# Performance work log

Measured on AMD Instinct MI355X. Metric: run time of the kernel, lower is better.

Reference implementation:

```python
import jax, jax.numpy as jnp
import numpy as np

D_MODEL = 1024
N_HEADS = 16
HEAD_DIM = D_MODEL // N_HEADS
D_FF = 4096
BATCH = 4
SEQ = 2048
LN_EPS = 1e-5


def layer_norm(x, g, b):
    mu = jnp.mean(x, axis=-1, keepdims=True)
    var = jnp.mean(jnp.square(x - mu), axis=-1, keepdims=True)
    return (x - mu) * jax.lax.rsqrt(var + LN_EPS) * g + b


def setup_inputs() -> dict:
    key = jax.random.key(0)
    ks = jax.random.split(key, 8)
    s = 0.02
    x = jax.random.normal(ks[0], (BATCH, SEQ, D_MODEL), jnp.float32)
    mask = jnp.triu(jnp.ones((SEQ, SEQ), dtype=bool), k=1)  # True = masked
    return {
        "x": x,
        "ln1_g": jnp.ones((D_MODEL,), jnp.float32),
        "ln1_b": jnp.zeros((D_MODEL,), jnp.float32),
        "qkv_w": jax.random.normal(ks[1], (3 * D_MODEL, D_MODEL), jnp.float32) * s,
        "qkv_b": jnp.zeros((3 * D_MODEL,), jnp.float32),
        "out_w": jax.random.normal(ks[2], (D_MODEL, D_MODEL), jnp.float32) * s,
        "out_b": jnp.zeros((D_MODEL,), jnp.float32),
        "ln2_g": jnp.ones((D_MODEL,), jnp.float32),
        "ln2_b": jnp.zeros((D_MODEL,), jnp.float32),
        "fc1_w": jax.random.normal(ks[3], (D_FF, D_MODEL), jnp.float32) * s,
        "fc1_b": jnp.zeros((D_FF,), jnp.float32),
        "fc2_w": jax.random.normal(ks[4], (D_MODEL, D_FF), jnp.float32) * s,
        "fc2_b": jnp.zeros((D_MODEL,), jnp.float32),
        "mask": mask,
    }


def reference(x, ln1_g, ln1_b, qkv_w, qkv_b, out_w, out_b,
              ln2_g, ln2_b, fc1_w, fc1_b, fc2_w, fc2_b, mask):
    b, s, _ = x.shape
    # --- pre-norm attention ---
    h = layer_norm(x, ln1_g, ln1_b)
    qkv = h @ qkv_w.T + qkv_b                       # [b, s, 3*D]
    qkv = qkv.reshape(b, s, 3, N_HEADS, HEAD_DIM)
    q, k, v = (jnp.moveaxis(qkv[:, :, i], 2, 1) for i in range(3))  # [b, H, s, hd]
    scale = HEAD_DIM ** -0.5
    attn = jnp.einsum('bhqd,bhkd->bhqk', q, k) * scale
    attn = jnp.where(mask, -jnp.inf, attn)
    attn = jax.nn.softmax(attn, axis=-1)
    o = jnp.einsum('bhqk,bhkd->bhqd', attn, v)      # [b, H, s, hd]
    o = jnp.moveaxis(o, 1, 2).reshape(b, s, D_MODEL)
    x = x + (o @ out_w.T + out_b)
    # --- pre-norm FFN ---
    h = layer_norm(x, ln2_g, ln2_b)
    h = jax.nn.gelu(h @ fc1_w.T + fc1_b, approximate=False)
    x = x + (h @ fc2_w.T + fc2_b)
    return x
```

## Files before the change

### kernel.cpp

```cpp
#include <hip/hip_runtime.h>
#include <math.h>

using u16 = unsigned short;
typedef __attribute__((ext_vector_type(8))) short short8;
typedef __attribute__((ext_vector_type(4))) float f32x4;
typedef __attribute__((ext_vector_type(16))) float f32x16;
typedef __attribute__((ext_vector_type(4))) u16 u16x4;

#define DEV __device__ __forceinline__

DEV u16 f2bf(float f) {
    unsigned u = __float_as_uint(f);
    u += 0x7fffu + ((u >> 16) & 1u);
    return (u16)(u >> 16);
}
DEV float bf2f(u16 h) { return __uint_as_float(((unsigned)h) << 16); }

DEV short8 ld16(const u16* p) { return *reinterpret_cast<const short8*>(p); }

DEV float gelu_f(float x) {
    const float u = x * (0.7978845608f + 0.0356774081f * x * x);
    const float e = __builtin_amdgcn_exp2f(u * 2.885390082f);
    const float t = 1.f - 2.f * __builtin_amdgcn_rcpf(e + 1.f);
    return 0.5f * x * (1.f + t);
}

DEV unsigned pk2(float a, float b) {
    unsigned r;
    asm("v_cvt_pk_bf16_f32 %0, %1, %2" : "=v"(r) : "v"(a), "v"(b));
    return r;
}

#define GLL16(gp, lp)                                                          \
    __builtin_amdgcn_global_load_lds(                                          \
        (const __attribute__((address_space(1))) void*)(gp),                   \
        (__attribute__((address_space(3))) void*)(lp), 16, 0, 0)

#define VMC(n) asm volatile("s_waitcnt vmcnt(" #n ")" ::: "memory")
#define LGKM0() asm volatile("s_waitcnt lgkmcnt(0)" ::: "memory")

__global__ void cvt_f32_bf16(const float* __restrict__ in, u16* __restrict__ out, int n4) {
    int i = blockIdx.x * 256 + threadIdx.x;
    if (i >= n4) return;
    float4 v = reinterpret_cast<const float4*>(in)[i];
    u16x4 o;
    o.x = f2bf(v.x); o.y = f2bf(v.y); o.z = f2bf(v.z); o.w = f2bf(v.w);
    reinterpret_cast<u16x4*>(out)[i] = o;
}

__global__ __launch_bounds__(256) void ln_bf16(const float* __restrict__ x,
                                               const float* __restrict__ gm,
                                               const float* __restrict__ bt,
                                               u16* __restrict__ out) {
    const int row = blockIdx.x, tid = threadIdx.x;
    const float4 v = reinterpret_cast<const float4*>(x + (long)row * 1024)[tid];
    float s  = v.x + v.y + v.z + v.w;
    float sq = v.x * v.x + v.y * v.y + v.z * v.z + v.w * v.w;
#pragma unroll
    for (int off = 1; off <= 32; off <<= 1) {
        s  += __shfl_xor(s, off);
        sq += __shfl_xor(sq, off);
    }
    __shared__ float ss[4], ssq[4];
    const int wave = tid >> 6, lane = tid & 63;
    if (lane == 0) { ss[wave] = s; ssq[wave] = sq; }
    __syncthreads();
    s  = ss[0] + ss[1] + ss[2] + ss[3];
    sq = ssq[0] + ssq[1] + ssq[2] + ssq[3];
    const float mu   = s * (1.f / 1024.f);
    const float var  = sq * (1.f / 1024.f) - mu * mu;
    const float rstd = rsqrtf(var + 1e-5f);
    const float4 g4 = reinterpret_cast<const float4*>(gm)[tid];
    const float4 b4 = reinterpret_cast<const float4*>(bt)[tid];
    u16x4 o;
    o.x = f2bf((v.x - mu) * rstd * g4.x + b4.x);
    o.y = f2bf((v.y - mu) * rstd * g4.y + b4.y);
    o.z = f2bf((v.z - mu) * rstd * g4.z + b4.z);
    o.w = f2bf((v.w - mu) * rstd * g4.w + b4.w);
    reinterpret_cast<u16x4*>(out + (long)row * 1024)[tid] = o;
}

#define TS(c, r) ((c) * 128 + (((((r) >> 3) ^ ((c) & 15))) << 3) + ((r) & 7))
#define CS(r, ck) ((r) * 128 + ((((ck) ^ ((r) & 15))) << 3))

template <int EPI, int BK>
__global__ __launch_bounds__(256, (BK == 32) ? 4 : 2) void gemm_bt(
    const u16* __restrict__ A, const u16* __restrict__ B,
    const float* __restrict__ bias, const float* res, float* outf,
    u16* __restrict__ outb, u16* __restrict__ Qb, u16* __restrict__ Kb,
    u16* __restrict__ Vtb, int M, int N, int K, int ldk) {
    constexpr int BUFU = (BK == 32) ? 8192 : 16384;
    __shared__ u16 shpool[2 * BUFU];

    const int tid = threadIdx.x;
    const int wave = tid >> 6, lane = tid & 63;
    const int lo = lane & 15, g = lane >> 4;
    const int wr = wave >> 1, wc = wave & 1;

    const int nwg = gridDim.x, chunk = nwg >> 3;
    const int wgid = (blockIdx.x & 7) * chunk + (blockIdx.x >> 3);
    const int nSmCol = N >> 10;
    const int s = wgid >> 6, w6 = wgid & 63;
    const int bm = (s / nSmCol) * 8 + (w6 >> 3);
    const int bn = (s % nSmCol) * 8 + (w6 & 7);
    const int row0 = bm * 128, col0 = bn * 128;

    const u16 *Ag, *Bg;
    if constexpr (BK == 32) {
        const int lrow = lane >> 2;
        const int lg   = (lane & 3) ^ ((lane >> 3) & 3);
        Ag = A + (long)(row0 + wave * 16 + lrow) * ldk + lg * 8;
        Bg = B + (long)(col0 + wave * 16 + lrow) * ldk + lg * 8;
    } else {
        const int lg = (lane & 7) ^ ((lane >> 3) & 7);
        Ag = A + (long)(row0 + wave * 32 + (lane >> 3)) * ldk + lg * 8;
        Bg = B + (long)(col0 + wave * 32 + (lane >> 3)) * ldk + lg * 8;
    }

    auto STAGE = [&](int tb, int kt) {
        if constexpr (BK == 32) {
            u16* Al = shpool + tb * 8192 + wave * 512;
            u16* Bl = Al + 4096;
            GLL16(Ag + (long)kt * 32, Al);
            GLL16(Ag + 64 * (long)ldk + (long)kt * 32, Al + 2048);
            GLL16(Bg + (long)kt * 32, Bl);
            GLL16(Bg + 64 * (long)ldk + (long)kt * 32, Bl + 2048);
        } else {
            u16* Al = shpool + tb * 16384 + wave * 2048;
            u16* Bl = Al + 8192;
            GLL16(Ag + (long)kt * 64,                  Al);
            GLL16(Ag + (long)kt * 64 +  8 * (long)ldk, Al + 512);
            GLL16(Ag + (long)kt * 64 + 16 * (long)ldk, Al + 1024);
            GLL16(Ag + (long)kt * 64 + 24 * (long)ldk, Al + 1536);
            GLL16(Bg + (long)kt * 64,                  Bl);
            GLL16(Bg + (long)kt * 64 +  8 * (long)ldk, Bl + 512);
            GLL16(Bg + (long)kt * 64 + 16 * (long)ldk, Bl + 1024);
            GLL16(Bg + (long)kt * 64 + 24 * (long)ldk, Bl + 1536);
        }
    };

    f32x4 acc[4][4] = {};

    STAGE(0, 0);
    STAGE(1, 1);

    const int T = K / BK;
    for (int t = 0; t < T; ++t) {
        const int cur = t & 1;
        if (t + 1 < T) {
            if constexpr (BK == 32) { VMC(4); } else { VMC(8); }
        } else { VMC(0); }
        __builtin_amdgcn_s_barrier();
        const u16* As = shpool + cur * BUFU;
        const u16* Bs = As + BUFU / 2;
        if constexpr (BK == 32) {
            short8 af[4], bfr[4];
            const int agp = g ^ ((lo >> 1) & 3);
#pragma unroll
            for (int m = 0; m < 4; ++m)
                af[m] = ld16(&As[(wr * 64 + m * 16 + lo) * 32 + agp * 8]);
#pragma unroll
            for (int n = 0; n < 4; ++n)
                bfr[n] = ld16(&Bs[(wc * 64 + n * 16 + lo) * 32 + agp * 8]);
            LGKM0();
            __builtin_amdgcn_s_barrier();
            if (t + 2 < T) STAGE(cur, t + 2);
#pragma unroll
            for (int m = 0; m < 4; ++m)
#pragma unroll
                for (int n = 0; n < 4; ++n)
                    acc[m][n] = __builtin_amdgcn_mfma_f32_16x16x32_bf16(
                        bfr[n], af[m], acc[m][n], 0, 0, 0);
        } else {
            short8 af[2][4], bfr[2][4];
#pragma unroll
            for (int ks = 0; ks < 2; ++ks) {
                const int ch = ((ks * 4 + g) ^ (lo & 7)) * 8;
#pragma unroll
                for (int m = 0; m < 4; ++m)
                    af[ks][m] = ld16(&As[(wr * 64 + m * 16 + lo) * 64 + ch]);
#pragma unroll
                for (int n = 0; n < 4; ++n)
                    bfr[ks][n] = ld16(&Bs[(wc * 64 + n * 16 + lo) * 64 + ch]);
            }
            LGKM0();
            __builtin_amdgcn_s_barrier();
            if (t + 2 < T) STAGE(cur, t + 2);
#pragma unroll
            for (int ks = 0; ks < 2; ++ks)
#pragma unroll
                for (int m = 0; m < 4; ++m)
#pragma unroll
                    for (int n = 0; n < 4; ++n)
                        acc[m][n] = __builtin_amdgcn_mfma_f32_16x16x32_bf16(
                            bfr[ks][n], af[ks][m], acc[m][n], 0, 0, 0);
        }
    }

    if constexpr (EPI == 1) {
#pragma unroll
        for (int n = 0; n < 4; ++n) {
            const int cb = col0 + wc * 64 + n * 16 + g * 4;
            const float4 b4 = *reinterpret_cast<const float4*>(&bias[cb]);
            const int ch = wc * 8 + n * 2 + (g >> 1);
#pragma unroll
            for (int m = 0; m < 4; ++m) {
                const int r = wr * 64 + m * 16 + lo;
                u16x4 o = {f2bf(gelu_f(acc[m][n][0] + b4.x)),
                           f2bf(gelu_f(acc[m][n][1] + b4.y)),
                           f2bf(gelu_f(acc[m][n][2] + b4.z)),
                           f2bf(gelu_f(acc[m][n][3] + b4.w))};
                *reinterpret_cast<u16x4*>(&shpool[CS(r, ch) + (g & 1) * 4]) = o;
            }
        }
        __syncthreads();
        const int row = tid >> 1, hl = tid & 1;
        u16* drow = outb + (long)(row0 + row) * N + col0 + hl * 64;
        const int rk = row & 15;
#pragma unroll
        for (int i = 0; i < 8; ++i) {
            const int ck = hl * 8 + i;
            *reinterpret_cast<short8*>(drow + i * 8) =
                *reinterpret_cast<const short8*>(&shpool[row * 128 + ((ck ^ rk) << 3)]);
        }
        return;
    }

    if constexpr (EPI == 3) {
        const int part = col0 >> 10;
        if (part == 2) {
            __syncthreads();
#pragma unroll
            for (int n = 0; n < 4; ++n) {
                const int cb = wc * 64 + n * 16 + g * 4;
                const float4 b4 = *reinterpret_cast<const float4*>(&bias[col0 + cb]);
#pragma unroll
                for (int m = 0; m < 4; ++m) {
                    const int rl = wr * 64 + m * 16 + lo;
                    shpool[TS(cb + 0, rl)] = f2bf(acc[m][n][0] + b4.x);
                    shpool[TS(cb + 1, rl)] = f2bf(acc[m][n][1] + b4.y);
                    shpool[TS(cb + 2, rl)] = f2bf(acc[m][n][2] + b4.z);
                    shpool[TS(cb + 3, rl)] = f2bf(acc[m][n][3] + b4.w);
                }
            }
            __syncthreads();
            const int c = tid >> 1, hlf = tid & 1;
            const int dcol = (col0 - 2048) + c;
            const int head = dcol >> 6, d = dcol & 63;
            const int bb = row0 >> 11;
            u16* dst = Vtb + ((long)(bb * 16 + head) * 64 + d) * 2048 +
                       (row0 & 2047) + hlf * 64;
            const u16* srcb = shpool + c * 128;
#pragma unroll
            for (int i = 0; i < 8; ++i) {
                const int pc = (hlf * 8 + i) ^ (c & 15);
                *reinterpret_cast<short8*>(dst + i * 8) =
                    *reinterpret_cast<const short8*>(srcb + pc * 8);
            }
            return;
        }
        const float qs = (part == 0) ? 0.18033688f : 1.0f;
#pragma unroll
        for (int n = 0; n < 4; ++n) {
            const int cb = col0 + wc * 64 + n * 16 + g * 4;
            const float4 b4 = *reinterpret_cast<const float4*>(&bias[cb]);
            const int ch = wc * 8 + n * 2 + (g >> 1);
#pragma unroll
            for (int m = 0; m < 4; ++m) {
                const int r = wr * 64 + m * 16 + lo;
                u16x4 o = {f2bf((acc[m][n][0] + b4.x) * qs),
                           f2bf((acc[m][n][1] + b4.y) * qs),
                           f2bf((acc[m][n][2] + b4.z) * qs),
                           f2bf((acc[m][n][3] + b4.w) * qs)};
                *reinterpret_cast<u16x4*>(&shpool[CS(r, ch) + (g & 1) * 4]) = o;
            }
        }
        __syncthreads();
        const int row = tid >> 1, hl = tid & 1;
        const int headbase = (col0 & 1023) >> 6;
        const int head = headbase + hl;
        const int bb = row0 >> 11;
        const int srow = (row0 & 2047) + row;
        u16* drow = (part == 0 ? Qb : Kb) +
                    ((long)(bb * 16 + head) * 2048 + srow) * 64;
        const int rk = row & 15;
#pragma unroll
        for (int i = 0; i < 8; ++i) {
            const int ck = hl * 8 + i;
            *reinterpret_cast<short8*>(drow + i * 8) =
                *reinterpret_cast<const short8*>(&shpool[row * 128 + ((ck ^ rk) << 3)]);
        }
        return;
    }

#pragma unroll
    for (int n = 0; n < 4; ++n) {
        const int cb = col0 + wc * 64 + n * 16 + g * 4;
        const float4 b4 = *reinterpret_cast<const float4*>(&bias[cb]);
#pragma unroll
        for (int m = 0; m < 4; ++m) {
            const int r = row0 + wr * 64 + m * 16 + lo;
            const float4 rr = *reinterpret_cast<const float4*>(&res[(long)r * N + cb]);
            float4 o = {rr.x + acc[m][n][0] + b4.x, rr.y + acc[m][n][1] + b4.y,
                        rr.z + acc[m][n][2] + b4.z, rr.w + acc[m][n][3] + b4.w};
            *reinterpret_cast<float4*>(&outf[(long)r * N + cb]) = o;
        }
    }
}

__global__ __launch_bounds__(256) void attn_fwd32(
    const u16* __restrict__ Q, const u16* __restrict__ K,
    const u16* __restrict__ Vt, u16* __restrict__ O) {
    __shared__ u16 kvl[2][8192];
    const int bh = blockIdx.x;
    const int strip = 15 - blockIdx.y;
    const int wave = threadIdx.x >> 6, lane = threadIdx.x & 63;
    const int lq = lane & 31, hi = lane >> 5;
    const int qw = strip * 128 + wave * 32;

    const u16* Kg = K + (long)bh * 2048 * 64;
    const u16* Vg = Vt + (long)bh * 64 * 2048;
    const int bb = bh >> 4, h = bh & 15;
    const u16* Qp = Q + ((long)bh * 2048 + qw) * 64;

    const int srow = wave * 8 + (lane >> 3);
    const int sc   = (lane & 7) ^ (srow & 7);

#define ASTAGE(b, kt) do {                                                     \
        const long kvb = (long)(kt) * 64;                                      \
        GLL16(Kg + (kvb + srow) * 64 + sc * 8,        &kvl[b][wave * 512]);    \
        GLL16(Kg + (kvb + 32 + srow) * 64 + sc * 8,   &kvl[b][2048 + wave * 512]); \
        GLL16(Vg + (long)srow * 2048 + kvb + sc * 8,  &kvl[b][4096 + wave * 512]); \
        GLL16(Vg + (long)(32 + srow) * 2048 + kvb + sc * 8,                    \
              &kvl[b][6144 + wave * 512]);                                     \
    } while (0)

    short8 qf[4];
#pragma unroll
    for (int ks = 0; ks < 4; ++ks)
        qf[ks] = ld16(Qp + lq * 64 + ks * 16 + hi * 8);

    f32x16 o0 = {}, o1 = {};
    float m = -1e30f, l = 0.f;
    const int q_abs = qw + lq;
    const int my_end = qw + 32;
    const int T = 2 * (strip + 1);
    const int swp = lq & 7;

    ASTAGE(0, 0);
    ASTAGE(1, 1);

    for (int t = 0; t < T; ++t) {
        const int cur = t & 1;
        const int kv0 = t * 64;
        if (t + 1 < T) { VMC(4); } else { VMC(0); }
        __builtin_amdgcn_s_barrier();
        const bool active = (kv0 < my_end);
        f32x16 s0 = {}, s1 = {};
        short8 vf0[4], vf1[4];
        if (active) {
            const u16* Kb = &kvl[cur][0];
            __builtin_amdgcn_s_setprio(1);
#pragma unroll
            for (int ks = 0; ks < 4; ++ks)
                s0 = __builtin_amdgcn_mfma_f32_32x32x16_bf16(
                    ld16(Kb + lq * 64 + ((ks * 2 + hi) ^ swp) * 8), qf[ks], s0, 0, 0, 0);
#pragma unroll
            for (int ks = 0; ks < 4; ++ks)
                s1 = __builtin_amdgcn_mfma_f32_32x32x16_bf16(
                    ld16(Kb + 2048 + lq * 64 + ((ks * 2 + hi) ^ swp) * 8), qf[ks], s1, 0, 0, 0);
            __builtin_amdgcn_s_setprio(0);
            const u16* Vb = &kvl[cur][4096];
#pragma unroll
            for (int c = 0; c < 4; ++c) {
                vf0[c] = ld16(Vb + lq * 64 + ((c * 2 + hi) ^ swp) * 8);
                vf1[c] = ld16(Vb + 2048 + lq * 64 + ((c * 2 + hi) ^ swp) * 8);
            }
        }
        LGKM0();
        __builtin_amdgcn_s_barrier();
        if (t + 2 < T) ASTAGE(cur, t + 2);
        if (active) {
            float mt = -1e30f;
            if (kv0 + 64 >= my_end) {
#pragma unroll
                for (int r = 0; r < 16; ++r) {
                    const int kv = kv0 + (r & 3) + 8 * (r >> 2) + 4 * hi;
                    if (kv > q_abs) s0[r] = -1e30f;
                    mt = fmaxf(mt, s0[r]);
                    if (kv + 32 > q_abs) s1[r] = -1e30f;
                    mt = fmaxf(mt, s1[r]);
                }
            } else {
#pragma unroll
                for (int r = 0; r < 16; ++r)
                    mt = fmaxf(mt, fmaxf(s0[r], s1[r]));
            }
            mt = fmaxf(mt, __shfl_xor(mt, 32));

            if (!__all(mt <= m + 11.5f)) {
                const float mn = fmaxf(m, mt);
                const float corr = __builtin_amdgcn_exp2f(m - mn);
                m = mn;
                l *= corr;
                o0 *= corr; o1 *= corr;
            }
            float ps = 0.f;
#pragma unroll
            for (int r = 0; r < 16; ++r) {
                s0[r] = __builtin_amdgcn_exp2f(s0[r] - m); ps += s0[r];
                s1[r] = __builtin_amdgcn_exp2f(s1[r] - m); ps += s1[r];
            }
            l += ps;

            short8 pf[4];
#pragma unroll
            for (int c = 0; c < 4; ++c) {
                const f32x16& src = (c >> 1) ? s1 : s0;
                const int b = (c & 1) * 8;
                const unsigned A0 = pk2(src[b + 0], src[b + 1]);
                const unsigned A1 = pk2(src[b + 2], src[b + 3]);
                const unsigned B0 = pk2(src[b + 4], src[b + 5]);
                const unsigned B1 = pk2(src[b + 6], src[b + 7]);
                const unsigned S0 = hi ? A0 : B0;
                const unsigned S1 = hi ? A1 : B1;
                const unsigned R0 = (unsigned)__shfl_xor((int)S0, 32);
                const unsigned R1 = (unsigned)__shfl_xor((int)S1, 32);
                union { unsigned u[4]; short8 v; } fr;
                fr.u[0] = hi ? R0 : A0;
                fr.u[1] = hi ? R1 : A1;
                fr.u[2] = hi ? B0 : R0;
                fr.u[3] = hi ? B1 : R1;
                pf[c] = fr.v;
            }

            __builtin_amdgcn_s_setprio(1);
#pragma unroll
            for (int c = 0; c < 4; ++c) {
                o0 = __builtin_amdgcn_mfma_f32_32x32x16_bf16(
                    vf0[c], pf[c], o0, 0, 0, 0);
                o1 = __builtin_amdgcn_mfma_f32_32x32x16_bf16(
                    vf1[c], pf[c], o1, 0, 0, 0);
            }
            __builtin_amdgcn_s_setprio(0);
        }
    }
#undef ASTAGE

    l += __shfl_xor(l, 32);
    const float inv = 1.f / l;
    u16* Orow = O + ((long)(bb * 2048 + qw + lq)) * 1024 + h * 64;
#pragma unroll
    for (int k4 = 0; k4 < 4; ++k4) {
        u16x4 w0, w1;
#pragma unroll
        for (int j = 0; j < 4; ++j) {
            w0[j] = f2bf(o0[k4 * 4 + j] * inv);
            w1[j] = f2bf(o1[k4 * 4 + j] * inv);
        }
        *reinterpret_cast<u16x4*>(Orow + 8 * k4 + 4 * hi)      = w0;
        *reinterpret_cast<u16x4*>(Orow + 32 + 8 * k4 + 4 * hi) = w1;
    }
}

extern "C" void kernel_launch(void* const* d_in, const int* in_sizes, int n_in,
                              void* d_out, int out_size, void* d_ws, size_t ws_size,
                              hipStream_t stream) {
    const float* x      = (const float*)d_in[0];
    const float* ln1_g  = (const float*)d_in[1];
    const float* ln1_b  = (const float*)d_in[2];
    const float* qkv_w  = (const float*)d_in[3];
    const float* qkv_b  = (const float*)d_in[4];
    const float* out_w  = (const float*)d_in[5];
    const float* out_b  = (const float*)d_in[6];
    const float* ln2_g  = (const float*)d_in[7];
    const float* ln2_b  = (const float*)d_in[8];
    const float* fc1_w  = (const float*)d_in[9];
    const float* fc1_b  = (const float*)d_in[10];
    const float* fc2_w  = (const float*)d_in[11];
    const float* fc2_b  = (const float*)d_in[12];
    float* out = (float*)d_out;

    const size_t MB = 1024ull * 1024ull;
    if (ws_size < 120 * MB) return;
    char* ws = (char*)d_ws;
    u16* wqkv = (u16*)(ws + 0);
    u16* wout = (u16*)(ws + 6 * MB);
    u16* wfc1 = (u16*)(ws + 8 * MB);
    u16* wfc2 = (u16*)(ws + 16 * MB);
    u16* hbuf = (u16*)(ws + 24 * MB);
    u16* obuf = (u16*)(ws + 40 * MB);
    u16* Qb   = (u16*)(ws + 56 * MB);
    u16* Kb   = (u16*)(ws + 72 * MB);
    u16* Vtb  = (u16*)(ws + 88 * MB);
    u16* gbuf = (u16*)(ws + 56 * MB);

    cvt_f32_bf16<<<3072, 256, 0, stream>>>(qkv_w, wqkv, 3072 * 1024 / 4);
    cvt_f32_bf16<<<1024, 256, 0, stream>>>(out_w, wout, 1024 * 1024 / 4);
    cvt_f32_bf16<<<4096, 256, 0, stream>>>(fc1_w, wfc1, 4096 * 1024 / 4);
    cvt_f32_bf16<<<4096, 256, 0, stream>>>(fc2_w, wfc2, 1024 * 4096 / 4);

    ln_bf16<<<8192, 256, 0, stream>>>(x, ln1_g, ln1_b, hbuf);
    gemm_bt<3, 32><<<dim3(1536), 256, 0, stream>>>(hbuf, wqkv, qkv_b, nullptr,
                                                   nullptr, nullptr, Qb, Kb, Vtb,
                                                   8192, 3072, 1024, 1024);
    attn_fwd32<<<dim3(64, 16), 256, 0, stream>>>(Qb, Kb, Vtb, obuf);
    gemm_bt<2, 64><<<dim3(512), 256, 0, stream>>>(obuf, wout, out_b, x, out,
                                                  nullptr, nullptr, nullptr, nullptr,
                                                  8192, 1024, 1024, 1024);
    ln_bf16<<<8192, 256, 0, stream>>>(out, ln2_g, ln2_b, hbuf);
    gemm_bt<1, 32><<<dim3(2048), 256, 0, stream>>>(hbuf, wfc1, fc1_b, nullptr,
                                                   nullptr, gbuf, nullptr, nullptr,
                                                   nullptr, 8192, 4096, 1024, 1024);
    gemm_bt<2, 64><<<dim3(512), 256, 0, stream>>>(gbuf, wfc2, fc2_b, out, out,
                                                  nullptr, nullptr, nullptr, nullptr,
                                                  8192, 1024, 4096, 4096);
}
```

Baseline: 371.1 us.

## Triple-buffer BK=32 GEMM, merge weight conversions, write GELU output directly

Merges the four weight-conversion launches into one grid-stride kernel, which removes launch overhead. The BK=32 GEMM moves from two to three LDS buffers and drops the second barrier and the lgkm wait in its loop, letting the next tile's load overlap compute; occupancy is lowered to 3 workgroups. The FC1 GELU epilogue now writes 8-byte fragments straight to global memory instead of staging in LDS for coalesced 16-byte rows. The narrower stores and lower occupancy may offset the gains.

```diff
diff --git a/kernel.cpp b/kernel.cpp
--- a/kernel.cpp
+++ b/kernel.cpp
@@ -39,13 +39,23 @@
 #define VMC(n) asm volatile("s_waitcnt vmcnt(" #n ")" ::: "memory")
 #define LGKM0() asm volatile("s_waitcnt lgkmcnt(0)" ::: "memory")
 
-__global__ void cvt_f32_bf16(const float* __restrict__ in, u16* __restrict__ out, int n4) {
-    int i = blockIdx.x * 256 + threadIdx.x;
-    if (i >= n4) return;
-    float4 v = reinterpret_cast<const float4*>(in)[i];
-    u16x4 o;
-    o.x = f2bf(v.x); o.y = f2bf(v.y); o.z = f2bf(v.z); o.w = f2bf(v.w);
-    reinterpret_cast<u16x4*>(out)[i] = o;
+__global__ __launch_bounds__(256) void cvt_all(
+    const float* __restrict__ s0, const float* __restrict__ s1,
+    const float* __restrict__ s2, const float* __restrict__ s3,
+    u16* __restrict__ d0, u16* __restrict__ d1,
+    u16* __restrict__ d2, u16* __restrict__ d3) {
+    for (long i = (long)blockIdx.x * 256 + threadIdx.x; i < 3145728;
+         i += (long)gridDim.x * 256) {
+        const float* s; u16* d; long j = i;
+        if (j < 786432)       { s = s0; d = d0; }
+        else if (j < 1048576) { s = s1; d = d1; j -= 786432; }
+        else if (j < 2097152) { s = s2; d = d2; j -= 1048576; }
+        else                  { s = s3; d = d3; j -= 2097152; }
+        float4 v = reinterpret_cast<const float4*>(s)[j];
+        u16x4 o;
+        o.x = f2bf(v.x); o.y = f2bf(v.y); o.z = f2bf(v.z); o.w = f2bf(v.w);
+        reinterpret_cast<u16x4*>(d)[j] = o;
+    }
 }
 
 __global__ __launch_bounds__(256) void ln_bf16(const float* __restrict__ x,
@@ -84,13 +94,14 @@
 #define CS(r, ck) ((r) * 128 + ((((ck) ^ ((r) & 15))) << 3))
 
 template <int EPI, int BK>
-__global__ __launch_bounds__(256, (BK == 32) ? 4 : 2) void gemm_bt(
+__global__ __launch_bounds__(256, (BK == 32) ? 3 : 2) void gemm_bt(
     const u16* __restrict__ A, const u16* __restrict__ B,
     const float* __restrict__ bias, const float* res, float* outf,
     u16* __restrict__ outb, u16* __restrict__ Qb, u16* __restrict__ Kb,
     u16* __restrict__ Vtb, int M, int N, int K, int ldk) {
     constexpr int BUFU = (BK == 32) ? 8192 : 16384;
-    __shared__ u16 shpool[2 * BUFU];
+    constexpr int NBUF = (BK == 32) ? 3 : 2;
+    __shared__ u16 shpool[NBUF * BUFU];
 
     const int tid = threadIdx.x;
     const int wave = tid >> 6, lane = tid & 63;
@@ -145,15 +156,13 @@
     STAGE(1, 1);
 
     const int T = K / BK;
-    for (int t = 0; t < T; ++t) {
-        const int cur = t & 1;
-        if (t + 1 < T) {
-            if constexpr (BK == 32) { VMC(4); } else { VMC(8); }
-        } else { VMC(0); }
-        __builtin_amdgcn_s_barrier();
-        const u16* As = shpool + cur * BUFU;
-        const u16* Bs = As + BUFU / 2;
-        if constexpr (BK == 32) {
+    if constexpr (BK == 32) {
+        for (int t = 0; t < T; ++t) {
+            if (t + 1 < T) { VMC(4); } else { VMC(0); }
+            __builtin_amdgcn_s_barrier();
+            if (t + 2 < T) STAGE((t + 2) % 3, t + 2);
+            const u16* As = shpool + (t % 3) * 8192;
+            const u16* Bs = As + 4096;
             short8 af[4], bfr[4];
             const int agp = g ^ ((lo >> 1) & 3);
 #pragma unroll
@@ -162,31 +171,35 @@
 #pragma unroll
             for (int n = 0; n < 4; ++n)
                 bfr[n] = ld16(&Bs[(wc * 64 + n * 16 + lo) * 32 + agp * 8]);
+#pragma unroll
+            for (int m = 0; m < 4; ++m)
+#pragma unroll
+                for (int n = 0; n < 4; ++n)
+                    acc[m][n] = __builtin_amdgcn_mfma_f32_16x16x32_bf16(
+                        bfr[n], af[m], acc[m][n], 0, 0, 0);
+        }
+    } else {
+        for (int t = 0; t < T; ++t) {
+            const int cur = t & 1;
+            if (t + 1 < T) { VMC(8); } else { VMC(0); }
+            __builtin_amdgcn_s_barrier();
+            const u16* As = shpool + cur * BUFU;
+            const u16* Bs = As + BUFU / 2;
+            short8 af[2][4], bfr[2][4];
+#pragma unroll
+            for (int ks = 0; ks < 2; ++ks) {
+                const int ch = ((ks * 4 + g) ^ (lo & 7)) * 8;
+#pragma unroll
+                for (int m = 0; m < 4; ++m)
+                    af[ks][m] = ld16(&As[(wr * 64 + m * 16 + lo) * 64 + ch]);
+#pragma unroll
+                for (int n = 0; n < 4; ++n)
+                    bfr[ks][n] = ld16(&Bs[(wc * 64 + n * 16 + lo) * 64 + ch]);
+            }
             LGKM0();
             __builtin_amdgcn_s_barrier();
             if (t + 2 < T) STAGE(cur, t + 2);
 #pragma unroll
-            for (int m = 0; m < 4; ++m)
-#pragma unroll
-                for (int n = 0; n < 4; ++n)
-                    acc[m][n] = __builtin_amdgcn_mfma_f32_16x16x32_bf16(
-                        bfr[n], af[m], acc[m][n], 0, 0, 0);
-        } else {
-            short8 af[2][4], bfr[2][4];
-#pragma unroll
-            for (int ks = 0; ks < 2; ++ks) {
-                const int ch = ((ks * 4 + g) ^ (lo & 7)) * 8;
-#pragma unroll
-                for (int m = 0; m < 4; ++m)
-                    af[ks][m] = ld16(&As[(wr * 64 + m * 16 + lo) * 64 + ch]);
-#pragma unroll
-                for (int n = 0; n < 4; ++n)
-                    bfr[ks][n] = ld16(&Bs[(wc * 64 + n * 16 + lo) * 64 + ch]);
-            }
-            LGKM0();
-            __builtin_amdgcn_s_barrier();
-            if (t + 2 < T) STAGE(cur, t + 2);
-#pragma unroll
             for (int ks = 0; ks < 2; ++ks)
 #pragma unroll
                 for (int m = 0; m < 4; ++m)
@@ -202,34 +215,23 @@
         for (int n = 0; n < 4; ++n) {
             const int cb = col0 + wc * 64 + n * 16 + g * 4;
             const float4 b4 = *reinterpret_cast<const float4*>(&bias[cb]);
-            const int ch = wc * 8 + n * 2 + (g >> 1);
 #pragma unroll
             for (int m = 0; m < 4; ++m) {
-                const int r = wr * 64 + m * 16 + lo;
+                const int r = row0 + wr * 64 + m * 16 + lo;
                 u16x4 o = {f2bf(gelu_f(acc[m][n][0] + b4.x)),
                            f2bf(gelu_f(acc[m][n][1] + b4.y)),
                            f2bf(gelu_f(acc[m][n][2] + b4.z)),
                            f2bf(gelu_f(acc[m][n][3] + b4.w))};
-                *reinterpret_cast<u16x4*>(&shpool[CS(r, ch) + (g & 1) * 4]) = o;
-            }
-        }
+                *reinterpret_cast<u16x4*>(&outb[(long)r * N + cb]) = o;
+            }
+        }
+        return;
+    }
+
+    if constexpr (EPI == 3) {
         __syncthreads();
-        const int row = tid >> 1, hl = tid & 1;
-        u16* drow = outb + (long)(row0 + row) * N + col0 + hl * 64;
-        const int rk = row & 15;
-#pragma unroll
-        for (int i = 0; i < 8; ++i) {
-            const int ck = hl * 8 + i;
-            *reinterpret_cast<short8*>(drow + i * 8) =
-                *reinterpret_cast<const short8*>(&shpool[row * 128 + ((ck ^ rk) << 3)]);
-        }
-        return;
-    }
-
-    if constexpr (EPI == 3) {
         const int part = col0 >> 10;
         if (part == 2) {
-            __syncthreads();
 #pragma unroll
             for (int n = 0; n < 4; ++n) {
                 const int cb = wc * 64 + n * 16 + g * 4;
@@ -495,10 +497,8 @@
     u16* Vtb  = (u16*)(ws + 88 * MB);
     u16* gbuf = (u16*)(ws + 56 * MB);
 
-    cvt_f32_bf16<<<3072, 256, 0, stream>>>(qkv_w, wqkv, 3072 * 1024 / 4);
-    cvt_f32_bf16<<<1024, 256, 0, stream>>>(out_w, wout, 1024 * 1024 / 4);
-    cvt_f32_bf16<<<4096, 256, 0, stream>>>(fc1_w, wfc1, 4096 * 1024 / 4);
-    cvt_f32_bf16<<<4096, 256, 0, stream>>>(fc2_w, wfc2, 1024 * 4096 / 4);
+    cvt_all<<<dim3(2048), 256, 0, stream>>>(qkv_w, out_w, fc1_w, fc2_w,
+                                            wqkv, wout, wfc1, wfc2);
 
     ln_bf16<<<8192, 256, 0, stream>>>(x, ln1_g, ln1_b, hbuf);
     gemm_bt<3, 32><<<dim3(1536), 256, 0, stream>>>(hbuf, wqkv, qkv_b, nullptr,
```

After: 364.6 us. About the same (-1.7%).
